# Kernel tuning notes

Measured on AMD Instinct MI355X. Metric: run time of the kernel, lower is better.

## Reference

```python
import jax, jax.numpy as jnp
import numpy as np

EPS = 1e-6
NUM_HEADS = 4


def setup_inputs() -> dict:
    key = jax.random.key(0)
    ks = jax.random.split(key, 7)
    B, C, H, W = 4, 128, 64, 64
    x = jax.random.normal(ks[0], (B, C, H, W), dtype=jnp.float32)
    norm_w = jnp.ones((C,), dtype=jnp.float32)
    norm_b = jnp.zeros((C,), dtype=jnp.float32)
    # 1x1 convs stored as [out_ch, in_ch] matrices
    qkv_w = jax.random.normal(ks[1], (3 * C, C), dtype=jnp.float32) / np.sqrt(C)
    qkv_b = jnp.zeros((3 * C,), dtype=jnp.float32)
    proj_w = jax.random.normal(ks[2], (C, C), dtype=jnp.float32) / np.sqrt(C)
    proj_b = jnp.zeros((C,), dtype=jnp.float32)
    return {"x": x, "norm_w": norm_w, "norm_b": norm_b,
            "qkv_w": qkv_w, "qkv_b": qkv_b, "proj_w": proj_w, "proj_b": proj_b}


def reference(x, norm_w, norm_b, qkv_w, qkv_b, proj_w, proj_b):
    B, C, H, W = x.shape
    nh = NUM_HEADS
    dh = C // nh
    N = H * W

    # ChannelLayerNorm: stats over channel dim per spatial position
    mean = jnp.mean(x, axis=1, keepdims=True)
    var = jnp.mean(jnp.square(x - mean), axis=1, keepdims=True)  # unbiased=False
    h = (x - mean) * jax.lax.rsqrt(var + EPS)
    h = h * norm_w[None, :, None, None] + norm_b[None, :, None, None]

    # qkv 1x1 conv -> [B, 3C, H, W]
    qkv = jnp.einsum('oc,bchw->bohw', qkv_w, h) + qkv_b[None, :, None, None]
    qkv = qkv.reshape(B, 3, nh, dh, N)
    q, k, v = qkv[:, 0], qkv[:, 1], qkv[:, 2]  # each [B, nh, dh, N]

    scale = dh ** -0.5
    attn = jnp.einsum('bhcn,bhcm->bhnm', q, k) * scale  # [B, nh, N, N]
    attn = jax.nn.softmax(attn, axis=-1)
    h = jnp.einsum('bhnm,bhcm->bhcn', attn, v)  # [B, nh, dh, N]
    h = h.reshape(B, C, H, W)

    h = jnp.einsum('oc,bchw->bohw', proj_w, h) + proj_b[None, :, None, None]
    return x + h
```

## Files before the change

### kernel.cpp

```cpp
#include <hip/hip_runtime.h>
#include <hip/hip_bf16.h>
#include <math.h>

#define BB 4
#define CC 128
#define NH 4
#define DH 32
#define NN 4096
#define OC3 (3*CC)

typedef __attribute__((ext_vector_type(8))) short short8;
typedef __attribute__((ext_vector_type(4))) short short4v;
typedef __attribute__((ext_vector_type(4))) float float4v;

__device__ inline short f2bf(float f) {
    unsigned u = __builtin_bit_cast(unsigned, f);
    u += 0x7FFF + ((u >> 16) & 1);
    return (short)(u >> 16);
}
__device__ inline unsigned pk2bf(float a, float b) {
    __hip_bfloat162 h = __float22bfloat162_rn(make_float2(a, b));
    unsigned u; __builtin_memcpy(&u, &h, 4);
    return u;
}
__device__ inline float bf2f(short s) {
    unsigned u = ((unsigned)(unsigned short)s) << 16;
    return __builtin_bit_cast(float, u);
}

#define HS 136
__global__ __launch_bounds__(512, 4) void lnqkv_kernel(
        const float* __restrict__ x, const float* __restrict__ nw,
        const float* __restrict__ nb, const float* __restrict__ qw,
        const float* __restrict__ qbias,
        short* __restrict__ qT, short* __restrict__ kT, short* __restrict__ vv) {
    __shared__ short hT[64 * HS];
    __shared__ float red[16][64];
    __shared__ float mrs[2][64];
    int t = threadIdx.x;
    int n0g = blockIdx.x * 64;
    int b = n0g >> 12, n0 = n0g & (NN - 1);
    int nl = t & 63, cq = t >> 6;

    const float* xp = x + ((size_t)b * CC + cq * 16) * NN + n0 + nl;
    float xv[16];
    float s = 0.f, ss = 0.f;
    #pragma unroll
    for (int j = 0; j < 16; ++j) {
        xv[j] = xp[(size_t)j * NN];
        s += xv[j]; ss += xv[j] * xv[j];
    }
    red[cq][nl] = s; red[cq + 8][nl] = ss;
    __syncthreads();
    if (t < 64) {
        float s8 = 0.f, q8 = 0.f;
        #pragma unroll
        for (int j = 0; j < 8; ++j) { s8 += red[j][t]; q8 += red[j + 8][t]; }
        float mean = s8 * (1.0f / CC);
        float var  = q8 * (1.0f / CC) - mean * mean;
        mrs[0][t] = mean;
        mrs[1][t] = rsqrtf(var + 1e-6f);
    }
    __syncthreads();
    {
        float mean = mrs[0][nl], rsv = mrs[1][nl];
        #pragma unroll
        for (int j = 0; j < 16; j += 8) {
            union { short8 v; unsigned u[4]; } z;
            #pragma unroll
            for (int k = 0; k < 4; ++k) {
                int c = cq * 16 + j + 2 * k;
                float h0 = (xv[j + 2 * k]     - mean) * rsv * nw[c]     + nb[c];
                float h1 = (xv[j + 2 * k + 1] - mean) * rsv * nw[c + 1] + nb[c + 1];
                z.u[k] = pk2bf(h0, h1);
            }
            *(short8*)&hT[nl * HS + cq * 16 + j] = z.v;
        }
    }
    __syncthreads();

    int w = t >> 6, lane = t & 63;
    int lg = lane >> 4, ln = lane & 15;
    int type = blockIdx.y;
    int ow = w * 16;
    const float* wp = qw + (size_t)(type * CC + ow + ln) * CC;
    float4v a0 = {0,0,0,0}, a1 = {0,0,0,0}, a2 = {0,0,0,0}, a3 = {0,0,0,0};
    #pragma unroll
    for (int cs = 0; cs < 4; ++cs) {
        float4 wa = *(const float4*)(wp + cs * 32 + lg * 8);
        float4 wb = *(const float4*)(wp + cs * 32 + lg * 8 + 4);
        union { short8 v; unsigned u[4]; } af;
        af.u[0] = pk2bf(wa.x, wa.y); af.u[1] = pk2bf(wa.z, wa.w);
        af.u[2] = pk2bf(wb.x, wb.y); af.u[3] = pk2bf(wb.z, wb.w);
        const short* hp = &hT[cs * 32 + lg * 8];
        a0 = __builtin_amdgcn_mfma_f32_16x16x32_bf16(af.v, *(const short8*)&hp[(0  + ln) * HS], a0, 0, 0, 0);
        a1 = __builtin_amdgcn_mfma_f32_16x16x32_bf16(af.v, *(const short8*)&hp[(16 + ln) * HS], a1, 0, 0, 0);
        a2 = __builtin_amdgcn_mfma_f32_16x16x32_bf16(af.v, *(const short8*)&hp[(32 + ln) * HS], a2, 0, 0, 0);
        a3 = __builtin_amdgcn_mfma_f32_16x16x32_bf16(af.v, *(const short8*)&hp[(48 + ln) * HS], a3, 0, 0, 0);
    }
    int r0g = type * CC + ow + lg * 4;
    float b0 = qbias[r0g], b1 = qbias[r0g + 1], b2 = qbias[r0g + 2], b3 = qbias[r0g + 3];
    int hh = ow >> 5;
    int cb = ow & 31;
    float4v* accs[4] = {&a0, &a1, &a2, &a3};
    if (type == 0) {
        const float qs = 0.1767766952966369f * 1.4426950408889634f;
        size_t rowbase = (size_t)(b * NH + hh) * NN + n0;
        #pragma unroll
        for (int nsub = 0; nsub < 4; ++nsub) {
            float4v av = *accs[nsub];
            union { short4v v; unsigned u[2]; } z;
            z.u[0] = pk2bf((av.x + b0) * qs, (av.y + b1) * qs);
            z.u[1] = pk2bf((av.z + b2) * qs, (av.w + b3) * qs);
            *(short4v*)&qT[(rowbase + nsub * 16 + ln) * DH + cb + lg * 4] = z.v;
        }
    } else if (type == 1) {
        size_t rowbase = (size_t)(b * NH + hh) * NN + n0;
        #pragma unroll
        for (int nsub = 0; nsub < 4; ++nsub) {
            float4v av = *accs[nsub];
            union { short4v v; unsigned u[2]; } z;
            z.u[0] = pk2bf(av.x + b0, av.y + b1);
            z.u[1] = pk2bf(av.z + b2, av.w + b3);
            *(short4v*)&kT[(rowbase + nsub * 16 + ln) * DH + cb + lg * 4] = z.v;
        }
    } else {
        size_t cbase = (size_t)((b * NH + hh) * DH + cb + lg * 4);
        #pragma unroll
        for (int nsub = 0; nsub < 4; ++nsub) {
            float4v av = *accs[nsub];
            size_t col = (size_t)n0 + nsub * 16 + ln;
            vv[(cbase + 0) * NN + col] = f2bf(av.x + b0);
            vv[(cbase + 1) * NN + col] = f2bf(av.y + b1);
            vv[(cbase + 2) * NN + col] = f2bf(av.z + b2);
            vv[(cbase + 3) * NN + col] = f2bf(av.w + b3);
        }
    }
}

#define PS 72
union __align__(16) FlashSh {
    short pt[8 * 16 * PS];
    struct { short mo[3][8][64][8]; float ml[3][8][64]; } m;
};
__global__ __launch_bounds__(512, 2) void flash_kernel(
        const short* __restrict__ qT, const short* __restrict__ kT,
        const short* __restrict__ vv, short* __restrict__ aoT) {
    __shared__ FlashSh sh;
    int blk = blockIdx.x;
    int bh = blk >> 5;
    int qb = blk & 31;
    int b = bh >> 2, hh = bh & 3;
    int n0 = qb * 128;
    int t = threadIdx.x, w = t >> 6, lane = t & 63;
    int lg = lane >> 4, ln = lane & 15;
    int qg = w & 1;
    int split = w >> 1;

    const short* kbase = kT + (size_t)bh * NN * DH + lg * 8;
    const short* vb0 = vv + ((size_t)bh * DH + ln) * NN + lg * 8;
    const short* vb1 = vb0 + (size_t)16 * NN;

    short8 qf[4];
    #pragma unroll
    for (int j = 0; j < 4; ++j)
        qf[j] = *(const short8*)&qT[((size_t)bh * NN + n0 + (qg * 4 + j) * 16 + ln) * DH + lg * 8];

    const short onebf = (short)0x3F80;
    short8 ones = {onebf, onebf, onebf, onebf, onebf, onebf, onebf, onebf};

    float4v o0[4], o1[4], lac[4];
    #pragma unroll
    for (int j = 0; j < 4; ++j) {
        o0[j] = (float4v){0,0,0,0}; o1[j] = (float4v){0,0,0,0};
        lac[j] = (float4v){0,0,0,0};
    }
    short* ptw = &sh.pt[w * 16 * PS];

    int mbeg = split * (NN / 4), mend = mbeg + NN / 4;
    for (int m0 = mbeg; m0 < mend; m0 += 64) {
        const short* kp = kbase + (size_t)m0 * DH;
        short8 k0 = *(const short8*)(kp + (size_t)(ln +  0) * DH);
        short8 k1 = *(const short8*)(kp + (size_t)(ln + 16) * DH);
        short8 k2 = *(const short8*)(kp + (size_t)(ln + 32) * DH);
        short8 k3 = *(const short8*)(kp + (size_t)(ln + 48) * DH);
        short8 v0 = *(const short8*)(vb0 + m0);
        short8 v1 = *(const short8*)(vb0 + m0 + 32);
        short8 v2 = *(const short8*)(vb1 + m0);
        short8 v3 = *(const short8*)(vb1 + m0 + 32);

        #pragma unroll
        for (int j = 0; j < 4; ++j) {
            float4v s0 = {0,0,0,0}, s1 = s0, s2 = s0, s3 = s0;
            s0 = __builtin_amdgcn_mfma_f32_16x16x32_bf16(k0, qf[j], s0, 0, 0, 0);
            s1 = __builtin_amdgcn_mfma_f32_16x16x32_bf16(k1, qf[j], s1, 0, 0, 0);
            s2 = __builtin_amdgcn_mfma_f32_16x16x32_bf16(k2, qf[j], s2, 0, 0, 0);
            s3 = __builtin_amdgcn_mfma_f32_16x16x32_bf16(k3, qf[j], s3, 0, 0, 0);
            float4v* sv[4] = {&s0, &s1, &s2, &s3};
            #pragma unroll
            for (int jj = 0; jj < 4; ++jj) {
                float4v sj = *sv[jj];
                float p0 = __builtin_amdgcn_exp2f(sj.x);
                float p1 = __builtin_amdgcn_exp2f(sj.y);
                float p2 = __builtin_amdgcn_exp2f(sj.z);
                float p3 = __builtin_amdgcn_exp2f(sj.w);
                union { short4v v; unsigned u[2]; } z;
                z.u[0] = pk2bf(p0, p1); z.u[1] = pk2bf(p2, p3);
                *(short4v*)&ptw[ln * PS + jj * 16 + lg * 4] = z.v;
            }
            short8 pb0 = *(const short8*)&ptw[ln * PS + 0  + lg * 8];
            short8 pb1 = *(const short8*)&ptw[ln * PS + 32 + lg * 8];
            o0[j]  = __builtin_amdgcn_mfma_f32_16x16x32_bf16(v0, pb0, o0[j], 0, 0, 0);
            o1[j]  = __builtin_amdgcn_mfma_f32_16x16x32_bf16(v2, pb0, o1[j], 0, 0, 0);
            lac[j] = __builtin_amdgcn_mfma_f32_16x16x32_bf16(ones, pb0, lac[j], 0, 0, 0);
            o0[j]  = __builtin_amdgcn_mfma_f32_16x16x32_bf16(v1, pb1, o0[j], 0, 0, 0);
            o1[j]  = __builtin_amdgcn_mfma_f32_16x16x32_bf16(v3, pb1, o1[j], 0, 0, 0);
            lac[j] = __builtin_amdgcn_mfma_f32_16x16x32_bf16(ones, pb1, lac[j], 0, 0, 0);
        }
    }

    __syncthreads();
    if (split > 0) {
        int si = split - 1;
        #pragma unroll
        for (int j = 0; j < 4; ++j) {
            int tid = qg * 4 + j;
            union { short8 v; unsigned u[4]; } z;
            z.u[0] = pk2bf(o0[j].x, o0[j].y);
            z.u[1] = pk2bf(o0[j].z, o0[j].w);
            z.u[2] = pk2bf(o1[j].x, o1[j].y);
            z.u[3] = pk2bf(o1[j].z, o1[j].w);
            *(short8*)&sh.m.mo[si][tid][lane][0] = z.v;
            sh.m.ml[si][tid][lane] = lac[j].x;
        }
    }
    __syncthreads();
    if (split == 0) {
        #pragma unroll
        for (int j = 0; j < 4; ++j) {
            int tid = qg * 4 + j;
            float lt = lac[j].x;
            #pragma unroll
            for (int si = 0; si < 3; ++si) {
                short8 q = *(const short8*)&sh.m.mo[si][tid][lane][0];
                o0[j].x += bf2f(q[0]); o0[j].y += bf2f(q[1]);
                o0[j].z += bf2f(q[2]); o0[j].w += bf2f(q[3]);
                o1[j].x += bf2f(q[4]); o1[j].y += bf2f(q[5]);
                o1[j].z += bf2f(q[6]); o1[j].w += bf2f(q[7]);
                lt += sh.m.ml[si][tid][lane];
            }
            float inv = 1.0f / lt;
            short* ap = aoT + ((size_t)b * NN + n0 + tid * 16 + ln) * CC + hh * DH;
            union { short4v v; unsigned u[2]; } z;
            z.u[0] = pk2bf(o0[j].x * inv, o0[j].y * inv);
            z.u[1] = pk2bf(o0[j].z * inv, o0[j].w * inv);
            *(short4v*)&ap[lg * 4] = z.v;
            z.u[0] = pk2bf(o1[j].x * inv, o1[j].y * inv);
            z.u[1] = pk2bf(o1[j].z * inv, o1[j].w * inv);
            *(short4v*)&ap[16 + lg * 4] = z.v;
        }
    }
}

__global__ __launch_bounds__(256) void proj_kernel(
        const short* __restrict__ aoT, const float* __restrict__ pw,
        const float* __restrict__ pb, const float* __restrict__ x,
        float* __restrict__ out) {
    int t = threadIdx.x;
    int n0g = blockIdx.x * 64;
    int b = n0g >> 12, n0 = n0g & (NN - 1);
    int o0 = blockIdx.y * 64;
    int wo = t >> 6, lane = t & 63;
    int lg = lane >> 4, ln = lane & 15;
    int ow = o0 + wo * 16;
    const float* wp = pw + (size_t)(ow + ln) * CC;
    const short* ap = aoT + (size_t)n0g * CC + lg * 8;
    float4v a0 = {0,0,0,0}, a1 = {0,0,0,0}, a2 = {0,0,0,0}, a3 = {0,0,0,0};
    #pragma unroll
    for (int cs = 0; cs < 4; ++cs) {
        float4 wa = *(const float4*)(wp + cs * 32 + lg * 8);
        float4 wb = *(const float4*)(wp + cs * 32 + lg * 8 + 4);
        union { short8 v; unsigned u[4]; } af;
        af.u[0] = pk2bf(wa.x, wa.y); af.u[1] = pk2bf(wa.z, wa.w);
        af.u[2] = pk2bf(wb.x, wb.y); af.u[3] = pk2bf(wb.z, wb.w);
        const short* hp = ap + cs * 32;
        a0 = __builtin_amdgcn_mfma_f32_16x16x32_bf16(af.v, *(const short8*)&hp[(size_t)(0  + ln) * CC], a0, 0, 0, 0);
        a1 = __builtin_amdgcn_mfma_f32_16x16x32_bf16(af.v, *(const short8*)&hp[(size_t)(16 + ln) * CC], a1, 0, 0, 0);
        a2 = __builtin_amdgcn_mfma_f32_16x16x32_bf16(af.v, *(const short8*)&hp[(size_t)(32 + ln) * CC], a2, 0, 0, 0);
        a3 = __builtin_amdgcn_mfma_f32_16x16x32_bf16(af.v, *(const short8*)&hp[(size_t)(48 + ln) * CC], a3, 0, 0, 0);
    }
    int r0 = ow + lg * 4;
    float b0 = pb[r0], b1 = pb[r0 + 1], b2 = pb[r0 + 2], b3 = pb[r0 + 3];
    const float* xbase = x   + ((size_t)b * CC + r0) * NN + n0 + ln;
    float*       obase = out + ((size_t)b * CC + r0) * NN + n0 + ln;
    float4v* accs[4] = {&a0, &a1, &a2, &a3};
    #pragma unroll
    for (int nsub = 0; nsub < 4; ++nsub) {
        float4v av = *accs[nsub];
        const float* xp = xbase + nsub * 16;
        float* op = obase + nsub * 16;
        op[(size_t)0 * NN] = av.x + b0 + xp[(size_t)0 * NN];
        op[(size_t)1 * NN] = av.y + b1 + xp[(size_t)1 * NN];
        op[(size_t)2 * NN] = av.z + b2 + xp[(size_t)2 * NN];
        op[(size_t)3 * NN] = av.w + b3 + xp[(size_t)3 * NN];
    }
}

extern "C" void kernel_launch(void* const* d_in, const int* in_sizes, int n_in,
                              void* d_out, int out_size, void* d_ws, size_t ws_size,
                              hipStream_t stream) {
    const float* x    = (const float*)d_in[0];
    const float* nw   = (const float*)d_in[1];
    const float* nb   = (const float*)d_in[2];
    const float* qkvw = (const float*)d_in[3];
    const float* qkvb = (const float*)d_in[4];
    const float* pw   = (const float*)d_in[5];
    const float* pb   = (const float*)d_in[6];
    float* out = (float*)d_out;

    short* qT  = (short*)d_ws;
    short* kT  = qT + (size_t)BB * NH * NN * DH;
    short* vv  = kT + (size_t)BB * NH * NN * DH;
    short* aoT = vv + (size_t)BB * NH * DH * NN;

    lnqkv_kernel<<<dim3(256, 3), 512, 0, stream>>>(x, nw, nb, qkvw, qkvb, qT, kT, vv);
    flash_kernel<<<dim3(512), 512, 0, stream>>>(qT, kT, vv, aoT);
    proj_kernel<<<dim3(256, 2), 256, 0, stream>>>(aoT, pw, pb, x, out);
}
```

Measured before the change: 155.5 us.

## Split flash attention KV range 8 ways and compute row sums on VALU

```diff
diff --git a/kernel.cpp b/kernel.cpp
--- a/kernel.cpp
+++ b/kernel.cpp
@@ -141,21 +141,20 @@
 #define PS 72
 union __align__(16) FlashSh {
     short pt[8 * 16 * PS];
-    struct { short mo[3][8][64][8]; float ml[3][8][64]; } m;
+    struct { short mo[7][4][64][8]; float ml[7][4][64]; } m;
 };
 __global__ __launch_bounds__(512, 2) void flash_kernel(
         const short* __restrict__ qT, const short* __restrict__ kT,
         const short* __restrict__ vv, short* __restrict__ aoT) {
     __shared__ FlashSh sh;
     int blk = blockIdx.x;
-    int bh = blk >> 5;
-    int qb = blk & 31;
+    int bh = blk >> 6;
+    int qb = blk & 63;
     int b = bh >> 2, hh = bh & 3;
-    int n0 = qb * 128;
+    int n0 = qb * 64;
     int t = threadIdx.x, w = t >> 6, lane = t & 63;
     int lg = lane >> 4, ln = lane & 15;
-    int qg = w & 1;
-    int split = w >> 1;
+    int split = w;
 
     const short* kbase = kT + (size_t)bh * NN * DH + lg * 8;
     const short* vb0 = vv + ((size_t)bh * DH + ln) * NN + lg * 8;
@@ -164,20 +163,17 @@
     short8 qf[4];
     #pragma unroll
     for (int j = 0; j < 4; ++j)
-        qf[j] = *(const short8*)&qT[((size_t)bh * NN + n0 + (qg * 4 + j) * 16 + ln) * DH + lg * 8];
-
-    const short onebf = (short)0x3F80;
-    short8 ones = {onebf, onebf, onebf, onebf, onebf, onebf, onebf, onebf};
-
-    float4v o0[4], o1[4], lac[4];
+        qf[j] = *(const short8*)&qT[((size_t)bh * NN + n0 + j * 16 + ln) * DH + lg * 8];
+
+    float4v o0[4], o1[4];
+    float ls[4];
     #pragma unroll
     for (int j = 0; j < 4; ++j) {
-        o0[j] = (float4v){0,0,0,0}; o1[j] = (float4v){0,0,0,0};
-        lac[j] = (float4v){0,0,0,0};
+        o0[j] = (float4v){0,0,0,0}; o1[j] = (float4v){0,0,0,0}; ls[j] = 0.f;
     }
     short* ptw = &sh.pt[w * 16 * PS];
 
-    int mbeg = split * (NN / 4), mend = mbeg + NN / 4;
+    int mbeg = split * (NN / 8), mend = mbeg + NN / 8;
     for (int m0 = mbeg; m0 < mend; m0 += 64) {
         const short* kp = kbase + (size_t)m0 * DH;
         short8 k0 = *(const short8*)(kp + (size_t)(ln +  0) * DH);
@@ -196,6 +192,7 @@
             s1 = __builtin_amdgcn_mfma_f32_16x16x32_bf16(k1, qf[j], s1, 0, 0, 0);
             s2 = __builtin_amdgcn_mfma_f32_16x16x32_bf16(k2, qf[j], s2, 0, 0, 0);
             s3 = __builtin_amdgcn_mfma_f32_16x16x32_bf16(k3, qf[j], s3, 0, 0, 0);
+            float lacc = 0.f;
             float4v* sv[4] = {&s0, &s1, &s2, &s3};
             #pragma unroll
             for (int jj = 0; jj < 4; ++jj) {
@@ -204,18 +201,18 @@
                 float p1 = __builtin_amdgcn_exp2f(sj.y);
                 float p2 = __builtin_amdgcn_exp2f(sj.z);
                 float p3 = __builtin_amdgcn_exp2f(sj.w);
+                lacc += (p0 + p1) + (p2 + p3);
                 union { short4v v; unsigned u[2]; } z;
                 z.u[0] = pk2bf(p0, p1); z.u[1] = pk2bf(p2, p3);
                 *(short4v*)&ptw[ln * PS + jj * 16 + lg * 4] = z.v;
             }
+            ls[j] += lacc;
             short8 pb0 = *(const short8*)&ptw[ln * PS + 0  + lg * 8];
             short8 pb1 = *(const short8*)&ptw[ln * PS + 32 + lg * 8];
-            o0[j]  = __builtin_amdgcn_mfma_f32_16x16x32_bf16(v0, pb0, o0[j], 0, 0, 0);
-            o1[j]  = __builtin_amdgcn_mfma_f32_16x16x32_bf16(v2, pb0, o1[j], 0, 0, 0);
-            lac[j] = __builtin_amdgcn_mfma_f32_16x16x32_bf16(ones, pb0, lac[j], 0, 0, 0);
-            o0[j]  = __builtin_amdgcn_mfma_f32_16x16x32_bf16(v1, pb1, o0[j], 0, 0, 0);
-            o1[j]  = __builtin_amdgcn_mfma_f32_16x16x32_bf16(v3, pb1, o1[j], 0, 0, 0);
-            lac[j] = __builtin_amdgcn_mfma_f32_16x16x32_bf16(ones, pb1, lac[j], 0, 0, 0);
+            o0[j] = __builtin_amdgcn_mfma_f32_16x16x32_bf16(v0, pb0, o0[j], 0, 0, 0);
+            o1[j] = __builtin_amdgcn_mfma_f32_16x16x32_bf16(v2, pb0, o1[j], 0, 0, 0);
+            o0[j] = __builtin_amdgcn_mfma_f32_16x16x32_bf16(v1, pb1, o0[j], 0, 0, 0);
+            o1[j] = __builtin_amdgcn_mfma_f32_16x16x32_bf16(v3, pb1, o1[j], 0, 0, 0);
         }
     }
 
@@ -224,33 +221,33 @@
         int si = split - 1;
         #pragma unroll
         for (int j = 0; j < 4; ++j) {
-            int tid = qg * 4 + j;
             union { short8 v; unsigned u[4]; } z;
             z.u[0] = pk2bf(o0[j].x, o0[j].y);
             z.u[1] = pk2bf(o0[j].z, o0[j].w);
             z.u[2] = pk2bf(o1[j].x, o1[j].y);
             z.u[3] = pk2bf(o1[j].z, o1[j].w);
-            *(short8*)&sh.m.mo[si][tid][lane][0] = z.v;
-            sh.m.ml[si][tid][lane] = lac[j].x;
+            *(short8*)&sh.m.mo[si][j][lane][0] = z.v;
+            sh.m.ml[si][j][lane] = ls[j];
         }
     }
     __syncthreads();
     if (split == 0) {
         #pragma unroll
         for (int j = 0; j < 4; ++j) {
-            int tid = qg * 4 + j;
-            float lt = lac[j].x;
+            float lt = ls[j];
             #pragma unroll
-            for (int si = 0; si < 3; ++si) {
-                short8 q = *(const short8*)&sh.m.mo[si][tid][lane][0];
+            for (int si = 0; si < 7; ++si) {
+                short8 q = *(const short8*)&sh.m.mo[si][j][lane][0];
                 o0[j].x += bf2f(q[0]); o0[j].y += bf2f(q[1]);
                 o0[j].z += bf2f(q[2]); o0[j].w += bf2f(q[3]);
                 o1[j].x += bf2f(q[4]); o1[j].y += bf2f(q[5]);
                 o1[j].z += bf2f(q[6]); o1[j].w += bf2f(q[7]);
-                lt += sh.m.ml[si][tid][lane];
+                lt += sh.m.ml[si][j][lane];
             }
+            lt += __shfl_xor(lt, 16, 64);
+            lt += __shfl_xor(lt, 32, 64);
             float inv = 1.0f / lt;
-            short* ap = aoT + ((size_t)b * NN + n0 + tid * 16 + ln) * CC + hh * DH;
+            short* ap = aoT + ((size_t)b * NN + n0 + j * 16 + ln) * CC + hh * DH;
             union { short4v v; unsigned u[2]; } z;
             z.u[0] = pk2bf(o0[j].x * inv, o0[j].y * inv);
             z.u[1] = pk2bf(o0[j].z * inv, o0[j].w * inv);
@@ -324,6 +321,6 @@
     short* aoT = vv + (size_t)BB * NH * DH * NN;
 
     lnqkv_kernel<<<dim3(256, 3), 512, 0, stream>>>(x, nw, nb, qkvw, qkvb, qT, kT, vv);
-    flash_kernel<<<dim3(512), 512, 0, stream>>>(qT, kT, vv, aoT);
+    flash_kernel<<<dim3(1024), 512, 0, stream>>>(qT, kT, vv, aoT);
     proj_kernel<<<dim3(256, 2), 256, 0, stream>>>(aoT, pw, pb, x, out);
 }
```

New measurement: 147.6 us. 1.05x faster.
